# Optimization experiments

Measured on AMD Instinct MI355X. Metric: run time of the kernel, lower is better.

Reference implementation:

```python
import jax, jax.numpy as jnp
import numpy as np


def setup_inputs() -> dict:
    key = jax.random.key(0)
    ks = jax.random.split(key, 5)
    B, N, D = 8, 2048, 512
    return {
        "query": jax.random.normal(ks[0], (B, N, D), dtype=jnp.float32),
        "key": jax.random.normal(ks[1], (B, N, D), dtype=jnp.float32),
        "value": jax.random.normal(ks[2], (B, N, D), dtype=jnp.float32),
        "w_k": jax.random.normal(ks[3], (2 * N - 1, D), dtype=jnp.float32),
        "w_v": jax.random.normal(ks[4], (2 * N - 1, D), dtype=jnp.float32),
    }


def reference(query, key, value, w_k, w_v):
    B, N, D = query.shape
    # skew indices: idx[i, j] = (N-1) - i + j  maps (i,j) -> relative distance j-i,
    # distance 0 sits at the middle column (N-1) of the 2N-1 relative table.
    idx = (N - 1) - jnp.arange(N)[:, None] + jnp.arange(N)[None, :]  # [N, N]

    # content scores: [B, N, N]
    base_scores = jnp.einsum("bqd,bkd->bqk", query, key)
    # relative key scores: matmul against full 2N-1 table then skewed gather
    all_rel = jnp.einsum("bqd,rd->bqr", query, w_k)  # [B, N, 2N-1]
    rel_scores = jnp.take_along_axis(
        all_rel, jnp.broadcast_to(idx[None], (B, N, N)), axis=-1
    )
    p_attn = jax.nn.softmax(base_scores + rel_scores, axis=-1)  # [B, N, N]

    # value path: scatter probabilities into skewed [B, N, 2N-1] layout,
    # then one matmul against the relative value table (equivalent to
    # sum_j p[i,j] * w_v[(N-1)-i+j]).
    rows = jnp.arange(N)[:, None]  # [N, 1] broadcast against idx [N, N]
    p_skew = jnp.zeros((B, N, 2 * N - 1), dtype=p_attn.dtype)
    p_skew = p_skew.at[:, rows, idx].set(p_attn)
    rel_out = jnp.einsum("bqr,rd->bqd", p_skew, w_v)

    out = jnp.einsum("bqk,bkd->bqd", p_attn, value) + rel_out
    return out, p_attn
```

## Files before the change

kernel.cpp:

```cpp
#include <hip/hip_runtime.h>


#define SEQN 2048
#define DD   512
#define NB   8
#define WROWS 4095
#define WPAD  4096

typedef float     f32x4 __attribute__((ext_vector_type(4)));
typedef _Float16  h16x4 __attribute__((ext_vector_type(4)));
typedef _Float16  h16x8 __attribute__((ext_vector_type(8)));

__device__ __forceinline__ unsigned swzw(int row, int c4) {
  unsigned b = (unsigned)(row * 64 + c4 * 8);
  return b ^ (((unsigned)row & 6u) << 3);
}
__device__ __forceinline__ unsigned swzr(int row, int kg) {
  unsigned b = (unsigned)(row * 64 + kg * 16);
  return b ^ (((unsigned)row & 6u) << 3);
}

typedef const __attribute__((address_space(1))) unsigned int gu32_t;
typedef __attribute__((address_space(3))) unsigned int lu32_t;
__device__ __forceinline__ void gload_lds16(const void* g, void* l) {
  __builtin_amdgcn_global_load_lds((gu32_t*)g, (lu32_t*)l, 16, 0, 0);
}

template <class P>
__device__ __forceinline__ void stage_tile(const P& prov, char* smem, int buf,
                                           int t, int wave, int l4, int cp) {
  char* lb = smem + buf * 16384;
#pragma unroll
  for (int h = 0; h < 2; h++) {
    int R = wave * 32 + h * 16;
    int row = R + l4;
    int c = cp ^ ((row >> 1) & 3);
    gload_lds16((const char*)prov.a_src(t, row) + c * 16, lb + R * 64);
    gload_lds16((const char*)prov.b_src(t, row) + c * 16, lb + 8192 + R * 64);
  }
}

template <int NT, class P>
__device__ __forceinline__ void gemm_core_cnt(const P& prov, char* smem, f32x4 (&acc)[4][4]) {
  const int tid = threadIdx.x;
  const int lane = tid & 63, wave = tid >> 6;
  const int l4 = lane >> 2, cp = lane & 3;
  const int wm = wave >> 1, wn = wave & 1;
  const int r16 = lane & 15, kg = lane >> 4;

  stage_tile(prov, smem, 0, 0, wave, l4, cp);
  stage_tile(prov, smem, 1, 1, wave, l4, cp);
  stage_tile(prov, smem, 2, 2, wave, l4, cp);

  int buf = 0;
  for (int t = 0; t < NT; t++) {
    asm volatile("s_waitcnt vmcnt(8)" ::: "memory");
    __builtin_amdgcn_s_barrier();
    char* lb = smem + buf * 16384;
    h16x8 af[4], bf[4];
#pragma unroll
    for (int mf = 0; mf < 4; mf++)
      af[mf] = *(const h16x8*)(lb + swzr(wm * 64 + mf * 16 + r16, kg));
#pragma unroll
    for (int nf = 0; nf < 4; nf++)
      bf[nf] = *(const h16x8*)(lb + 8192 + swzr(wn * 64 + nf * 16 + r16, kg));
#pragma unroll
    for (int mf = 0; mf < 4; mf++)
#pragma unroll
      for (int nf = 0; nf < 4; nf++)
        acc[mf][nf] = __builtin_amdgcn_mfma_f32_16x16x32_f16(af[mf], bf[nf], acc[mf][nf], 0, 0, 0);
    asm volatile("s_waitcnt lgkmcnt(0)" ::: "memory");
    __builtin_amdgcn_s_barrier();
    int nt2 = t + 3; if (nt2 >= NT) nt2 = NT - 1;
    stage_tile(prov, smem, buf, nt2, wave, l4, cp);
    buf = (buf == 2) ? 0 : buf + 1;
  }
}

struct ProvQK {
  const char *ar, *br;
  __device__ __forceinline__ const void* a_src(int t, int row) const {
    return ar + (size_t)row * 1024 + (size_t)t * 64;
  }
  __device__ __forceinline__ const void* b_src(int t, int row) const {
    return br + (size_t)row * 1024 + (size_t)t * 64;
  }
};
struct ProvRel {
  const char *ar, *wk; int tb;
  __device__ __forceinline__ const void* a_src(int t, int row) const {
    return ar + (size_t)row * 1024 + (size_t)t * 64;
  }
  __device__ __forceinline__ const void* b_src(int t, int row) const {
    int tr = tb + row; if (tr > WROWS - 1) tr = WROWS - 1;
    return wk + (size_t)tr * 1024 + (size_t)t * 64;
  }
};

__global__ __launch_bounds__(256) void cvt_f16_k(const float* __restrict__ in,
                                                 _Float16* __restrict__ out, long n8) {
  for (long i = (long)blockIdx.x * 256 + threadIdx.x; i < n8; i += (long)gridDim.x * 256) {
    f32x4 a = ((const f32x4*)in)[i * 2];
    f32x4 b = ((const f32x4*)in)[i * 2 + 1];
    h16x8 h = {(_Float16)a[0], (_Float16)a[1], (_Float16)a[2], (_Float16)a[3],
               (_Float16)b[0], (_Float16)b[1], (_Float16)b[2], (_Float16)b[3]};
    ((h16x8*)out)[i] = h;
  }
}

__global__ __launch_bounds__(256) void transpose_v_k(const float* __restrict__ v,
                                                     _Float16* __restrict__ vT) {
  __shared__ float tile[32][33];
  const int d0 = blockIdx.x * 32, j0 = blockIdx.y * 32, b = blockIdx.z;
  const int tid = threadIdx.x;
#pragma unroll
  for (int rep = 0; rep < 4; rep++) {
    int idx = rep * 256 + tid;
    int rr = idx >> 5, cc = idx & 31;
    tile[rr][cc] = v[((size_t)(b * SEQN + j0 + rr)) * DD + d0 + cc];
  }
  __syncthreads();
#pragma unroll
  for (int rep = 0; rep < 4; rep++) {
    int idx = rep * 256 + tid;
    int rr = idx >> 5, cc = idx & 31;
    vT[((size_t)(b * DD + d0 + rr)) * SEQN + j0 + cc] = (_Float16)tile[cc][rr];
  }
}

__global__ __launch_bounds__(256) void transpose_wv_k(const float* __restrict__ wv,
                                                      _Float16* __restrict__ wvT) {
  __shared__ float tile[32][33];
  const int d0 = blockIdx.x * 32, r0 = blockIdx.y * 32;
  const int tid = threadIdx.x;
#pragma unroll
  for (int rep = 0; rep < 4; rep++) {
    int idx = rep * 256 + tid;
    int rr = idx >> 5, cc = idx & 31;
    float val = 0.f;
    if (r0 + rr < WROWS) val = wv[(size_t)(r0 + rr) * DD + d0 + cc];
    tile[rr][cc] = val;
  }
  __syncthreads();
#pragma unroll
  for (int rep = 0; rep < 4; rep++) {
    int idx = rep * 256 + tid;
    int rr = idx >> 5, cc = idx & 31;
    wvT[(size_t)(d0 + rr) * WPAD + r0 + cc] = (_Float16)tile[cc][rr];
  }
}

__global__ __launch_bounds__(256) void score_base2_k(const _Float16* __restrict__ qh,
                                                     const _Float16* __restrict__ kh,
                                                     float* __restrict__ S) {
  __shared__ __align__(16) char smem[49152];
  const int j0 = blockIdx.x * 128, i0 = blockIdx.y * 128, b = blockIdx.z;
  const int tid = threadIdx.x, lane = tid & 63, wave = tid >> 6;
  const int wm = wave >> 1, wn = wave & 1, r16 = lane & 15, kg = lane >> 4;

  f32x4 acc[4][4];
#pragma unroll
  for (int mf = 0; mf < 4; mf++)
#pragma unroll
    for (int nf = 0; nf < 4; nf++) acc[mf][nf] = (f32x4){0.f, 0.f, 0.f, 0.f};

  ProvQK prov{(const char*)(qh + (size_t)(b * SEQN + i0) * DD),
              (const char*)(kh + (size_t)(b * SEQN + j0) * DD)};
  gemm_core_cnt<16>(prov, smem, acc);

#pragma unroll
  for (int mf = 0; mf < 4; mf++)
#pragma unroll
    for (int nf = 0; nf < 4; nf++)
#pragma unroll
      for (int r = 0; r < 4; r++) {
        int ii = wm * 64 + mf * 16 + kg * 4 + r;
        int jj = wn * 64 + nf * 16 + r16;
        S[(size_t)(b * SEQN + i0 + ii) * SEQN + j0 + jj] = acc[mf][nf][r];
      }
}

__global__ __launch_bounds__(256) void score_rel2_k(const _Float16* __restrict__ qh,
                                                    const _Float16* __restrict__ wkh,
                                                    float* __restrict__ S) {
  __shared__ __align__(16) char smem[49152];
  const int z = blockIdx.x, i0 = blockIdx.y * 128, b = blockIdx.z;
  const int tid = threadIdx.x, lane = tid & 63, wave = tid >> 6;
  const int wm = wave >> 1, wn = wave & 1, r16 = lane & 15, kg = lane >> 4;
  const int tmin = SEQN - 128 - i0;

  f32x4 acc[4][4];
#pragma unroll
  for (int mf = 0; mf < 4; mf++)
#pragma unroll
    for (int nf = 0; nf < 4; nf++) acc[mf][nf] = (f32x4){0.f, 0.f, 0.f, 0.f};

  ProvRel prov{(const char*)(qh + (size_t)(b * SEQN + i0) * DD),
               (const char*)wkh, tmin + z * 128};
  gemm_core_cnt<16>(prov, smem, acc);

#pragma unroll
  for (int mf = 0; mf < 4; mf++)
#pragma unroll
    for (int nf = 0; nf < 4; nf++) {
      int bcg = z * 128 + wn * 64 + nf * 16 + r16;
#pragma unroll
      for (int r = 0; r < 4; r++) {
        int ii = wm * 64 + mf * 16 + kg * 4 + r;
        int j = bcg + ii - 127;
        if (bcg <= 2174 && j >= 0 && j < SEQN)
          S[(size_t)(b * SEQN + i0 + ii) * SEQN + j] += acc[mf][nf][r];
      }
    }
}

__global__ __launch_bounds__(256) void softmax_rows_k(float* __restrict__ S) {
  const int wid = threadIdx.x >> 6, lane = threadIdx.x & 63;
  const size_t row = (size_t)blockIdx.x * 4 + wid;
  float* p = S + row * SEQN;
  f32x4 x[8];
  float m = -3.4e38f;
#pragma unroll
  for (int c = 0; c < 8; c++) {
    x[c] = *(const f32x4*)(p + c * 256 + lane * 4);
    m = fmaxf(m, fmaxf(fmaxf(x[c][0], x[c][1]), fmaxf(x[c][2], x[c][3])));
  }
#pragma unroll
  for (int off = 32; off > 0; off >>= 1) m = fmaxf(m, __shfl_xor(m, off));
  float s = 0.f;
#pragma unroll
  for (int c = 0; c < 8; c++)
#pragma unroll
    for (int e = 0; e < 4; e++) {
      x[c][e] = __expf(x[c][e] - m);
      s += x[c][e];
    }
#pragma unroll
  for (int off = 32; off > 0; off >>= 1) s += __shfl_xor(s, off);
  float inv = 1.f / s;
#pragma unroll
  for (int c = 0; c < 8; c++) {
    x[c][0] *= inv; x[c][1] *= inv; x[c][2] *= inv; x[c][3] *= inv;
    *(f32x4*)(p + c * 256 + lane * 4) = x[c];
  }
}

__global__ __launch_bounds__(512) void out_gemm9_k(const float* __restrict__ S,
                                                   const _Float16* __restrict__ vT,
                                                   const _Float16* __restrict__ wvT,
                                                   float* __restrict__ outp) {
  __shared__ __align__(16) char smem[49152];
  const int bid = blockIdx.x;
  const int xcd = bid & 7, rr = bid >> 3;
  const int x = rr & 3, s8 = rr >> 2;
  const int rt = xcd + 8 * s8;
  const int d0 = x * 128, b = rt >> 3, i0 = (rt & 7) * 256;
  const int tid = threadIdx.x, lane = tid & 63, wave = tid >> 6;
  const int wm = wave >> 1, wn = wave & 1, r16 = lane & 15, kg = lane >> 4;
  const int tmin = SEQN - 256 - i0;

  const float*    pb = S  + (size_t)(b * SEQN + i0) * SEQN;
  const _Float16* vb = vT + (size_t)(b * DD + d0) * SEQN;
  const _Float16* wb = wvT + (size_t)d0 * WPAD + tmin;

  f32x4 acc[4][4];
#pragma unroll
  for (int mf = 0; mf < 4; mf++)
#pragma unroll
    for (int nf = 0; nf < 4; nf++) acc[mf][nf] = (f32x4){0.f, 0.f, 0.f, 0.f};

  f32x4 ra[4];
  h16x4 rbv[2];

  auto LOADREGS = [&](int t) {
    if (t < 64) {
      const int k0 = t * 32;
#pragma unroll
      for (int rep = 0; rep < 4; rep++) {
        int f = rep * 512 + tid, row = f >> 3, c4 = f & 7;
        ra[rep] = *(const f32x4*)(pb + (size_t)row * SEQN + k0 + c4 * 4);
      }
#pragma unroll
      for (int rep = 0; rep < 2; rep++) {
        int f = rep * 512 + tid, row = f >> 3, c4 = f & 7;
        rbv[rep] = *(const h16x4*)(vb + (size_t)row * SEQN + k0 + c4 * 4);
      }
    } else {
      const int k0 = (t - 64) * 32;
      const bool clean = (t >= 72) && (t < 128);
#pragma unroll
      for (int rep = 0; rep < 4; rep++) {
        int f = rep * 512 + tid, row = f >> 3, c4 = f & 7;
        int jb = k0 + c4 * 4 + row - 255;
        const float* pr = pb + (size_t)row * SEQN;
        f32x4 v4;
        if (clean) {
          __builtin_memcpy(&v4, pr + jb, 16);
        } else {
#pragma unroll
          for (int e = 0; e < 4; e++) {
            int j = jb + e;
            v4[e] = (j >= 0 && j < SEQN) ? pr[j] : 0.f;
          }
        }
        ra[rep] = v4;
      }
#pragma unroll
      for (int rep = 0; rep < 2; rep++) {
        int f = rep * 512 + tid, row = f >> 3, c4 = f & 7;
        rbv[rep] = *(const h16x4*)(wb + (size_t)row * WPAD + k0 + c4 * 4);
      }
    }
  };
  auto WRITE = [&](char* lb) {
#pragma unroll
    for (int rep = 0; rep < 4; rep++) {
      int f = rep * 512 + tid, row = f >> 3, c4 = f & 7;
      h16x4 ha = {(_Float16)ra[rep][0], (_Float16)ra[rep][1],
                  (_Float16)ra[rep][2], (_Float16)ra[rep][3]};
      *(h16x4*)(lb + swzw(row, c4)) = ha;
    }
#pragma unroll
    for (int rep = 0; rep < 2; rep++) {
      int f = rep * 512 + tid, row = f >> 3, c4 = f & 7;
      *(h16x4*)(lb + 16384 + swzw(row, c4)) = rbv[rep];
    }
  };

  LOADREGS(0);
  WRITE(smem);
  LOADREGS(1);
  __syncthreads();

  for (int t = 0; t < 136; t++) {
    char* lb = smem + (t & 1) * 24576;
    if (t + 1 < 136) WRITE(smem + ((t + 1) & 1) * 24576);
    h16x8 af[4], bf[4];
#pragma unroll
    for (int mf = 0; mf < 4; mf++)
      af[mf] = *(const h16x8*)(lb + swzr(wm * 64 + mf * 16 + r16, kg));
#pragma unroll
    for (int nf = 0; nf < 4; nf++)
      bf[nf] = *(const h16x8*)(lb + 16384 + swzr(wn * 64 + nf * 16 + r16, kg));
    if (t + 2 < 136) LOADREGS(t + 2);
#pragma unroll
    for (int mf = 0; mf < 4; mf++)
#pragma unroll
      for (int nf = 0; nf < 4; nf++)
        acc[mf][nf] = __builtin_amdgcn_mfma_f32_16x16x32_f16(af[mf], bf[nf], acc[mf][nf], 0, 0, 0);
    __syncthreads();
  }

#pragma unroll
  for (int mf = 0; mf < 4; mf++)
#pragma unroll
    for (int nf = 0; nf < 4; nf++)
#pragma unroll
      for (int r = 0; r < 4; r++) {
        int ii = wm * 64 + mf * 16 + kg * 4 + r;
        int dd = wn * 64 + nf * 16 + r16;
        outp[(size_t)(b * SEQN + i0 + ii) * DD + d0 + dd] = acc[mf][nf][r];
      }
}

extern "C" void kernel_launch(void* const* d_in, const int* in_sizes, int n_in,
                              void* d_out, int out_size, void* d_ws, size_t ws_size,
                              hipStream_t stream) {
  const float* q  = (const float*)d_in[0];
  const float* k  = (const float*)d_in[1];
  const float* v  = (const float*)d_in[2];
  const float* wk = (const float*)d_in[3];
  const float* wv = (const float*)d_in[4];

  float* outp = (float*)d_out;
  float* S    = outp + (size_t)NB * SEQN * DD;

  const size_t nVT = (size_t)NB * DD * SEQN;
  const size_t nWV = (size_t)DD * WPAD;
  const size_t nQH = (size_t)NB * SEQN * DD;
  _Float16* vT  = (_Float16*)d_ws;
  _Float16* wvT = vT + nVT;
  _Float16* qh  = wvT + nWV;
  _Float16* kh  = qh + nQH;
  _Float16* wkh = kh + nQH;

  cvt_f16_k<<<dim3(2048), 256, 0, stream>>>(q,  qh,  (long)(nQH / 8));
  cvt_f16_k<<<dim3(2048), 256, 0, stream>>>(k,  kh,  (long)(nQH / 8));
  cvt_f16_k<<<dim3(1024), 256, 0, stream>>>(wk, wkh, (long)((size_t)WROWS * DD / 8));
  transpose_v_k <<<dim3(DD / 32, SEQN / 32, NB), 256, 0, stream>>>(v, vT);
  transpose_wv_k<<<dim3(DD / 32, 128),           256, 0, stream>>>(wv, wvT);

  score_base2_k <<<dim3(SEQN / 128, SEQN / 128, NB), 256, 0, stream>>>(qh, kh, S);
  score_rel2_k  <<<dim3(17, SEQN / 128, NB),         256, 0, stream>>>(qh, wkh, S);
  softmax_rows_k<<<dim3(NB * SEQN / 4),              256, 0, stream>>>(S);
  out_gemm9_k   <<<dim3(256),                        512, 0, stream>>>(S, vT, wvT, outp);
}
```

Measured before the change: 405.9 us.

## Enlarge score GEMM tiles to 256x128 with 8-wave blocks sharing B tile

The base and relative score kernels now use 512-thread blocks covering 256 query rows by 128 columns, so each staged key/w_k tile is reused across twice as many query rows. The staging routine loads a 256-row A tile and a shared 128-row B tile per buffer, the LDS triple buffer grows to 72KB, and the wait count is adjusted for fewer loads per thread. The relative-score index offsets and grid are updated for the taller row block. This cuts B-operand global traffic per output, at the cost of fewer blocks and more LDS per block, which may lower occupancy.

New measurement: 430.9 us. +6.2%, slower.

```diff
diff --git a/kernel.cpp b/kernel.cpp
--- a/kernel.cpp
+++ b/kernel.cpp
@@ -27,43 +27,48 @@
 }
 
 template <class P>
-__device__ __forceinline__ void stage_tile(const P& prov, char* smem, int buf,
-                                           int t, int wave, int l4, int cp) {
-  char* lb = smem + buf * 16384;
+__device__ __forceinline__ void stage_tile8(const P& prov, char* smem, int buf,
+                                            int t, int wave, int l4, int cp) {
+  char* lb = smem + buf * 24576;
 #pragma unroll
   for (int h = 0; h < 2; h++) {
     int R = wave * 32 + h * 16;
     int row = R + l4;
     int c = cp ^ ((row >> 1) & 3);
     gload_lds16((const char*)prov.a_src(t, row) + c * 16, lb + R * 64);
-    gload_lds16((const char*)prov.b_src(t, row) + c * 16, lb + 8192 + R * 64);
+  }
+  {
+    int RB = wave * 16;
+    int rowb = RB + l4;
+    int cb = cp ^ ((rowb >> 1) & 3);
+    gload_lds16((const char*)prov.b_src(t, rowb) + cb * 16, lb + 16384 + RB * 64);
   }
 }
 
 template <int NT, class P>
-__device__ __forceinline__ void gemm_core_cnt(const P& prov, char* smem, f32x4 (&acc)[4][4]) {
+__device__ __forceinline__ void gemm_core8(const P& prov, char* smem, f32x4 (&acc)[4][4]) {
   const int tid = threadIdx.x;
   const int lane = tid & 63, wave = tid >> 6;
   const int l4 = lane >> 2, cp = lane & 3;
   const int wm = wave >> 1, wn = wave & 1;
   const int r16 = lane & 15, kg = lane >> 4;
 
-  stage_tile(prov, smem, 0, 0, wave, l4, cp);
-  stage_tile(prov, smem, 1, 1, wave, l4, cp);
-  stage_tile(prov, smem, 2, 2, wave, l4, cp);
+  stage_tile8(prov, smem, 0, 0, wave, l4, cp);
+  stage_tile8(prov, smem, 1, 1, wave, l4, cp);
+  stage_tile8(prov, smem, 2, 2, wave, l4, cp);
 
   int buf = 0;
   for (int t = 0; t < NT; t++) {
-    asm volatile("s_waitcnt vmcnt(8)" ::: "memory");
+    asm volatile("s_waitcnt vmcnt(6)" ::: "memory");
     __builtin_amdgcn_s_barrier();
-    char* lb = smem + buf * 16384;
+    char* lb = smem + buf * 24576;
     h16x8 af[4], bf[4];
 #pragma unroll
     for (int mf = 0; mf < 4; mf++)
       af[mf] = *(const h16x8*)(lb + swzr(wm * 64 + mf * 16 + r16, kg));
 #pragma unroll
     for (int nf = 0; nf < 4; nf++)
-      bf[nf] = *(const h16x8*)(lb + 8192 + swzr(wn * 64 + nf * 16 + r16, kg));
+      bf[nf] = *(const h16x8*)(lb + 16384 + swzr(wn * 64 + nf * 16 + r16, kg));
 #pragma unroll
     for (int mf = 0; mf < 4; mf++)
 #pragma unroll
@@ -72,7 +77,7 @@
     asm volatile("s_waitcnt lgkmcnt(0)" ::: "memory");
     __builtin_amdgcn_s_barrier();
     int nt2 = t + 3; if (nt2 >= NT) nt2 = NT - 1;
-    stage_tile(prov, smem, buf, nt2, wave, l4, cp);
+    stage_tile8(prov, smem, buf, nt2, wave, l4, cp);
     buf = (buf == 2) ? 0 : buf + 1;
   }
 }
@@ -150,11 +155,11 @@
   }
 }
 
-__global__ __launch_bounds__(256) void score_base2_k(const _Float16* __restrict__ qh,
+__global__ __launch_bounds__(512) void score_base3_k(const _Float16* __restrict__ qh,
                                                      const _Float16* __restrict__ kh,
                                                      float* __restrict__ S) {
-  __shared__ __align__(16) char smem[49152];
-  const int j0 = blockIdx.x * 128, i0 = blockIdx.y * 128, b = blockIdx.z;
+  __shared__ __align__(16) char smem[73728];
+  const int j0 = blockIdx.x * 128, i0 = blockIdx.y * 256, b = blockIdx.z;
   const int tid = threadIdx.x, lane = tid & 63, wave = tid >> 6;
   const int wm = wave >> 1, wn = wave & 1, r16 = lane & 15, kg = lane >> 4;
 
@@ -166,7 +171,7 @@
 
   ProvQK prov{(const char*)(qh + (size_t)(b * SEQN + i0) * DD),
               (const char*)(kh + (size_t)(b * SEQN + j0) * DD)};
-  gemm_core_cnt<16>(prov, smem, acc);
+  gemm_core8<16>(prov, smem, acc);
 
 #pragma unroll
   for (int mf = 0; mf < 4; mf++)
@@ -180,14 +185,14 @@
       }
 }
 
-__global__ __launch_bounds__(256) void score_rel2_k(const _Float16* __restrict__ qh,
+__global__ __launch_bounds__(512) void score_rel3_k(const _Float16* __restrict__ qh,
                                                     const _Float16* __restrict__ wkh,
                                                     float* __restrict__ S) {
-  __shared__ __align__(16) char smem[49152];
-  const int z = blockIdx.x, i0 = blockIdx.y * 128, b = blockIdx.z;
+  __shared__ __align__(16) char smem[73728];
+  const int z = blockIdx.x, i0 = blockIdx.y * 256, b = blockIdx.z;
   const int tid = threadIdx.x, lane = tid & 63, wave = tid >> 6;
   const int wm = wave >> 1, wn = wave & 1, r16 = lane & 15, kg = lane >> 4;
-  const int tmin = SEQN - 128 - i0;
+  const int tmin = SEQN - 256 - i0;
 
   f32x4 acc[4][4];
 #pragma unroll
@@ -197,7 +202,7 @@
 
   ProvRel prov{(const char*)(qh + (size_t)(b * SEQN + i0) * DD),
                (const char*)wkh, tmin + z * 128};
-  gemm_core_cnt<16>(prov, smem, acc);
+  gemm_core8<16>(prov, smem, acc);
 
 #pragma unroll
   for (int mf = 0; mf < 4; mf++)
@@ -207,8 +212,8 @@
 #pragma unroll
       for (int r = 0; r < 4; r++) {
         int ii = wm * 64 + mf * 16 + kg * 4 + r;
-        int j = bcg + ii - 127;
-        if (bcg <= 2174 && j >= 0 && j < SEQN)
+        int j = bcg + ii - 255;
+        if (bcg <= 2302 && j >= 0 && j < SEQN)
           S[(size_t)(b * SEQN + i0 + ii) * SEQN + j] += acc[mf][nf][r];
       }
     }
@@ -390,8 +395,8 @@
   transpose_v_k <<<dim3(DD / 32, SEQN / 32, NB), 256, 0, stream>>>(v, vT);
   transpose_wv_k<<<dim3(DD / 32, 128),           256, 0, stream>>>(wv, wvT);
 
-  score_base2_k <<<dim3(SEQN / 128, SEQN / 128, NB), 256, 0, stream>>>(qh, kh, S);
-  score_rel2_k  <<<dim3(17, SEQN / 128, NB),         256, 0, stream>>>(qh, wkh, S);
+  score_base3_k <<<dim3(SEQN / 128, SEQN / 256, NB), 512, 0, stream>>>(qh, kh, S);
+  score_rel3_k  <<<dim3(18, SEQN / 256, NB),         512, 0, stream>>>(qh, wkh, S);
   softmax_rows_k<<<dim3(NB * SEQN / 4),              256, 0, stream>>>(S);
   out_gemm9_k   <<<dim3(256),                        512, 0, stream>>>(S, vT, wvT, outp);
 }
```
